# Kernel optimization log

Hardware: AMD Instinct MI355X
Metric: run time of the kernel (lower is better)

The kernel has to match this reference:

```python
import jax, jax.numpy as jnp
import numpy as np

C, H2, E, SQ, SK, HW = 256, 256, 512, 2048, 64, 256

def setup_inputs() -> dict:
    key = jax.random.key(0)
    ks = jax.random.split(key, 12)
    s = 0.05
    return {
        "Z": jax.random.normal(ks[0], (C, HW, HW), jnp.float32),
        "Q": jax.random.normal(ks[1], (SQ, 3), jnp.float32),
        "q_z": jax.random.normal(ks[2], (SQ, C), jnp.float32),
        "r": jax.random.uniform(ks[3], (SQ, SK, 2), jnp.float32) * (HW - 2),
        "w1": jax.random.normal(ks[4], (H2, 2), jnp.float32) * s,
        "b1": jnp.zeros((H2,), jnp.float32),
        "w2": jax.random.normal(ks[5], (H2, 3), jnp.float32) * s,
        "b2": jnp.zeros((H2,), jnp.float32),
        "in_proj_w": jax.random.normal(ks[6], (3 * E, E), jnp.float32) * s,
        "in_proj_b": jnp.zeros((3 * E,), jnp.float32),
        "out_proj_w": jax.random.normal(ks[7], (E, E), jnp.float32) * s,
        "out_proj_b": jnp.zeros((E,), jnp.float32),
        "num_heads": 8,
    }

def bilinear_interpolation_3d(Z, x, y):
    # Z: [c, H, W]; x, y: [N] float coords. Faithful to torch: .int() trunc (coords >= 0)
    c = Z.shape[0]
    x1 = x.astype(jnp.int32)
    y1 = y.astype(jnp.int32)
    x2 = x1 + 1
    y2 = y1 + 1
    Q11 = Z[:, x1, y1]  # [c, N]
    Q12 = Z[:, x1, y2]
    Q21 = Z[:, x2, y1]
    Q22 = Z[:, x2, y2]
    dx = x - x1
    dy = y - y1
    R1 = Q11 * (1 - dx) + Q21 * dx
    R2 = Q12 * (1 - dx) + Q22 * dx
    interp = R1 * (1 - dy) + R2 * dy  # [c, N]
    # faithful to the original: raw row-major reshape (NOT a transpose)
    return jnp.reshape(interp, (-1, c))

def reference(Z, Q, q_z, r, w1, b1, w2, b2, in_proj_w, in_proj_b, out_proj_w, out_proj_b, num_heads):
    size_q, size_k, _ = r.shape
    qr = r.reshape(-1, 2)
    Zr = bilinear_interpolation_3d(Z, qr[:, 0], qr[:, 1])
    Zr = Zr.reshape(size_q, size_k, -1)  # [sq, sk, c]
    r_proj = r @ w1.T + b1               # [sq, sk, h2]
    key = jnp.concatenate([Zr, r_proj], axis=2)  # [sq, sk, E]
    value = key
    q_proj = Q @ w2.T + b2               # [sq, h2]
    query = jnp.concatenate([q_z, q_proj], axis=1)  # [sq, E]
    E_ = query.shape[1]
    hd = E_ // num_heads
    # torch MultiheadAttention in-projection
    ql = query @ in_proj_w[:E_].T + in_proj_b[:E_]              # [sq, E]
    kl = key @ in_proj_w[E_:2 * E_].T + in_proj_b[E_:2 * E_]    # [sq, sk, E]
    vl = value @ in_proj_w[2 * E_:].T + in_proj_b[2 * E_:]
    qh = ql.reshape(size_q, num_heads, hd)
    kh = kl.reshape(size_q, size_k, num_heads, hd)
    vh = vl.reshape(size_q, size_k, num_heads, hd)
    scores = jnp.einsum('bhd,bkhd->bhk', qh, kh) / jnp.sqrt(jnp.asarray(hd, qh.dtype))
    attn = jax.nn.softmax(scores, axis=-1)  # [sq, h, sk]
    out = jnp.einsum('bhk,bkhd->bhd', attn, vh).reshape(size_q, E_)
    out = out @ out_proj_w.T + out_proj_b
    return jnp.concatenate([q_z, out], axis=1)  # [sq, c + E]
```

## Files before the change

### kernel.cpp

```cpp
#include <hip/hip_runtime.h>


typedef _Float16 half8 __attribute__((ext_vector_type(8)));
typedef _Float16 half4v __attribute__((ext_vector_type(4)));
typedef _Float16 half2v __attribute__((ext_vector_type(2)));
typedef float f32x4 __attribute__((ext_vector_type(4)));

#define O_WQT   0u
#define O_WKT   262144u
#define O_WVT   524288u
#define O_WO    786432u
#define O_QRY   1048576u
#define O_WCT   2097152u
#define O_MT    4194304u
#define O_U     6291456u
#define O_G     14680064u
#define O_ZT    23068672u
#define O_ZR    39845888u
#define O_F32   73400320u

__global__ __launch_bounds__(256) void k_pre(
    const float* __restrict__ Z, const float* __restrict__ ipw,
    const float* __restrict__ opw, const float* __restrict__ q_z,
    const float* __restrict__ Qm, const float* __restrict__ w2,
    const float* __restrict__ b2, const float* __restrict__ ipb,
    const float* __restrict__ opb,
    _Float16* __restrict__ wsh, float* __restrict__ bu, float* __restrict__ b_eff)
{
    __shared__ __align__(16) float sbuf[8448];
    int b = blockIdx.x, t = threadIdx.x;

    if (b < 2048) {
        float (*sT)[33] = (float(*)[33])sbuf;
        int x = b >> 3, yt = (b & 7) * 32;
#pragma unroll
        for (int i = 0; i < 8; ++i) {
            int g = i * 256 + t;
            int c = g >> 3, y = (g & 7) * 4;
            float4 v = *(const float4*)(Z + (size_t)c * 65536 + x * 256 + yt + y);
            sT[c][y] = v.x; sT[c][y + 1] = v.y; sT[c][y + 2] = v.z; sT[c][y + 3] = v.w;
        }
        __syncthreads();
        _Float16* Zt = wsh + O_ZT;
        int c4 = (t & 63) * 4;
#pragma unroll
        for (int i = 0; i < 8; ++i) {
            int y = (t >> 6) * 8 + i;
            half4v o;
#pragma unroll
            for (int j = 0; j < 4; ++j) o[j] = (_Float16)sT[c4 + j][y];
            *(half4v*)(Zt + ((size_t)(x * 256 + yt + y)) * 256 + c4) = o;
        }
    } else if (b < 2240) {
        float (*sT)[65] = (float(*)[65])sbuf;
        int bx = b - 2048;
        int sec = bx >> 6, tile = bx & 63;
        int th = tile >> 3, tl = tile & 7;
        int row0, col0;
        if (sec == 0) { row0 = tl * 64;             col0 = th * 64; }
        else          { row0 = 512 * sec + th * 64; col0 = tl * 64; }
        const float* src = ipw + (size_t)row0 * 512 + col0;
#pragma unroll
        for (int i = 0; i < 4; ++i) {
            int rr = i * 16 + (t >> 4), cc = (t & 15) * 4;
            float4 v = *(const float4*)(src + (size_t)rr * 512 + cc);
            sT[rr][cc] = v.x; sT[rr][cc + 1] = v.y; sT[rr][cc + 2] = v.z; sT[rr][cc + 3] = v.w;
        }
        __syncthreads();
        float scale = (sec == 1) ? 0.125f : 1.0f;
#pragma unroll
        for (int it = 0; it < 2; ++it) {
            int g = t + it * 256;
            int a = g >> 3, b8 = (g & 7) * 8;
            half8 o;
#pragma unroll
            for (int j = 0; j < 8; ++j) o[j] = (_Float16)(scale * sT[b8 + j][a]);
            size_t dst;
            if (sec == 0)      dst = O_WQT + (size_t)(th * 64 + a) * 512 + tl * 64 + b8;
            else if (sec == 1) dst = O_WKT + (size_t)th * 32768 + (size_t)(tl * 64 + a) * 64 + b8;
            else               dst = O_WVT + (size_t)th * 32768 + (size_t)(tl * 64 + a) * 64 + b8;
            *(half8*)(wsh + dst) = o;
        }
    } else if (b < 3264) {
        int e4 = ((b - 2240) * 256 + t) * 4;
        int q = e4 >> 9, j = e4 & 511;
        half4v o;
        if (j < 256) {
            float4 v = *(const float4*)(q_z + q * 256 + j);
            o[0] = (_Float16)v.x; o[1] = (_Float16)v.y;
            o[2] = (_Float16)v.z; o[3] = (_Float16)v.w;
        } else {
            float q0 = Qm[q * 3], q1 = Qm[q * 3 + 1], q2 = Qm[q * 3 + 2];
#pragma unroll
            for (int u = 0; u < 4; ++u) {
                int m = j - 256 + u;
                o[u] = (_Float16)(q0 * w2[m * 3] + q1 * w2[m * 3 + 1] + q2 * w2[m * 3 + 2] + b2[m]);
            }
        }
        *(half4v*)(wsh + O_QRY + e4) = o;
    } else if (b < 3520) {
        int e4 = ((b - 3264) * 256 + t) * 4;
        float4 v = *(const float4*)(opw + e4);
        half4v o;
        o[0] = (_Float16)v.x; o[1] = (_Float16)v.y; o[2] = (_Float16)v.z; o[3] = (_Float16)v.w;
        *(half4v*)(wsh + O_WO + e4) = o;
    } else if (b < 3536) {
        int c = (b - 3520) * 256 + t;
        int h = c >> 9, j = c & 511;
        float s = 0.f;
#pragma unroll 4
        for (int d = 0; d < 64; ++d)
            s += ipb[512 + (h << 6) + d] * ipw[(size_t)(512 + (h << 6) + d) * 512 + j];
        bu[c] = 0.125f * s;
    } else {
        int e = (b - 3536) * 4 + (t >> 6), l = t & 63;
        const float* worow = opw + (size_t)e * 512;
        float s = 0.f;
#pragma unroll
        for (int i = 0; i < 8; ++i)
            s += ipb[1024 + l + 64 * i] * worow[l + 64 * i];
#pragma unroll
        for (int mm = 1; mm < 64; mm <<= 1) s += __shfl_xor(s, mm, 64);
        if (l == 0) b_eff[e] = s + opb[e];
    }
}

__global__ __launch_bounds__(256) void k_small2(_Float16* __restrict__ wsh)
{
    __shared__ __align__(16) _Float16 sA[64][72];
    int bx = blockIdx.x;
    int job = bx >> 6, g6 = bx & 63;
    int rb = g6 & 7, h = g6 >> 3;
    int t = threadIdx.x, w = t >> 6, l = t & 63;
    const _Float16* A0 = wsh + (job ? O_WO : O_WQT) + (size_t)rb * 64 * 512 + h * 64;
    const _Float16* B0 = wsh + (job ? O_WVT : O_WKT) + (size_t)h * 512 * 64;
#pragma unroll
    for (int i = 0; i < 2; ++i) {
        int g = t + i * 256;
        int row = g >> 3, colg = (g & 7) * 8;
        *(half8*)&sA[row][colg] = *(const half8*)(A0 + (size_t)row * 512 + colg);
    }
    __syncthreads();
    f32x4 acc[4][8] = {};
    int arow = l & 15, kg = (l >> 4) << 3;
#pragma unroll
    for (int kk = 0; kk < 64; kk += 32) {
        half8 a[4], bb[8];
#pragma unroll
        for (int mt = 0; mt < 4; ++mt) a[mt] = *(const half8*)&sA[mt * 16 + arow][kk + kg];
#pragma unroll
        for (int nt = 0; nt < 8; ++nt) {
            int col = (w << 7) + nt * 16 + arow;
            bb[nt] = *(const half8*)(B0 + (size_t)col * 64 + kk + kg);
        }
#pragma unroll
        for (int mt = 0; mt < 4; ++mt)
#pragma unroll
            for (int nt = 0; nt < 8; ++nt)
                acc[mt][nt] = __builtin_amdgcn_mfma_f32_16x16x32_f16(a[mt], bb[nt], acc[mt][nt], 0, 0, 0);
    }
    if (job == 0) {
        _Float16* C = wsh + O_WCT;
#pragma unroll
        for (int mt = 0; mt < 4; ++mt)
#pragma unroll
            for (int nt = 0; nt < 8; ++nt) {
                int col = (h << 9) + (w << 7) + nt * 16 + arow;
                int row0 = rb * 64 + mt * 16 + ((l >> 4) << 2);
#pragma unroll
                for (int v = 0; v < 4; ++v)
                    C[(size_t)col * 512 + row0 + v] = (_Float16)acc[mt][nt][v];
            }
    } else {
        _Float16* C0 = wsh + O_MT + (size_t)rb * 64 * 4096 + h * 512;
#pragma unroll
        for (int mt = 0; mt < 4; ++mt)
#pragma unroll
            for (int nt = 0; nt < 8; ++nt)
#pragma unroll
                for (int v = 0; v < 4; ++v) {
                    int row = mt * 16 + ((l >> 4) << 2) + v;
                    int col = (w << 7) + nt * 16 + arow;
                    C0[(size_t)row * 4096 + col] = (_Float16)acc[mt][nt][v];
                }
    }
}

__global__ __launch_bounds__(256, 4) void k_mid(
    const float* __restrict__ r, _Float16* __restrict__ wsh,
    const float* __restrict__ bu)
{
    __shared__ __align__(16) unsigned char smem[33792];
    int b = blockIdx.x, t = threadIdx.x, w = t >> 6, l = t & 63;

    if (b < 512) {
        _Float16 (*sA)[264] = (_Float16(*)[264])smem;
        const _Float16* A = wsh + O_QRY;
        const _Float16* B = wsh + O_WCT;
        _Float16* U = wsh + O_U;
        int q0 = (b & 31) * 64;
        int colb = (b >> 5) * 256 + w * 64;
        f32x4 acc[4][4] = {};
        int arow = l & 15, kg = (l >> 4) << 3;
#pragma unroll
        for (int half = 0; half < 2; ++half) {
#pragma unroll
            for (int i = 0; i < 8; ++i) {
                int e = i * 2048 + t * 8;
                *(half8*)&sA[e >> 8][e & 255] =
                    *(const half8*)(A + (size_t)(q0 + (e >> 8)) * 512 + half * 256 + (e & 255));
            }
            __syncthreads();
#pragma unroll 2
            for (int kk = 0; kk < 256; kk += 32) {
                half8 a[4], bb[4];
#pragma unroll
                for (int mt = 0; mt < 4; ++mt) a[mt] = *(const half8*)&sA[mt * 16 + arow][kk + kg];
#pragma unroll
                for (int nt = 0; nt < 4; ++nt)
                    bb[nt] = *(const half8*)(B + (size_t)(colb + nt * 16 + arow) * 512 + half * 256 + kk + kg);
#pragma unroll
                for (int mt = 0; mt < 4; ++mt)
#pragma unroll
                    for (int nt = 0; nt < 4; ++nt)
                        acc[mt][nt] = __builtin_amdgcn_mfma_f32_16x16x32_f16(a[mt], bb[nt], acc[mt][nt], 0, 0, 0);
            }
            __syncthreads();
        }
#pragma unroll
        for (int mt = 0; mt < 4; ++mt)
#pragma unroll
            for (int nt = 0; nt < 4; ++nt)
#pragma unroll
                for (int v = 0; v < 4; ++v) {
                    int row = q0 + mt * 16 + ((l >> 4) << 2) + v;
                    int col = colb + nt * 16 + arow;
                    U[(size_t)row * 4096 + col] = (_Float16)(acc[mt][nt][v] + bu[col]);
                }
    } else {
        float (*sT)[33] = (float(*)[33])smem;
        const _Float16* Zt = wsh + O_ZT;
        _Float16* Zr = wsh + O_ZR;
        int pb = b - 512;
        const float2* r2 = (const float2*)r;
#pragma unroll 2
        for (int i = 0; i < 8; ++i) {
            int ptl = w * 8 + i;
            float2 rv = r2[pb * 32 + ptl];
            int x1 = (int)rv.x, y1 = (int)rv.y;
            float dx = rv.x - (float)x1, dy = rv.y - (float)y1;
            float w11 = (1.f - dx) * (1.f - dy), w21 = dx * (1.f - dy);
            float w12 = (1.f - dx) * dy,         w22 = dx * dy;
            const _Float16* base = Zt + ((size_t)(x1 * 256 + y1)) * 256;
#pragma unroll
            for (int cg = 0; cg < 2; ++cg) {
                int c = cg * 128 + l * 2;
                half2v z11 = *(const half2v*)(base + c);
                half2v z12 = *(const half2v*)(base + 256 + c);
                half2v z21 = *(const half2v*)(base + 65536 + c);
                half2v z22 = *(const half2v*)(base + 65536 + 256 + c);
                sT[c][ptl]     = w11 * (float)z11[0] + w21 * (float)z21[0]
                               + w12 * (float)z12[0] + w22 * (float)z22[0];
                sT[c + 1][ptl] = w11 * (float)z11[1] + w21 * (float)z21[1]
                               + w12 * (float)z12[1] + w22 * (float)z22[1];
            }
        }
        __syncthreads();
        int ch0 = t >> 2, colc = (t & 3) * 8;
#pragma unroll
        for (int g = 0; g < 4; ++g) {
            int ch = g * 64 + ch0;
            half8 o;
#pragma unroll
            for (int j = 0; j < 8; ++j) o[j] = (_Float16)sT[ch][colc + j];
            *(half8*)(Zr + (size_t)ch * 131072 + pb * 32 + colc) = o;
        }
    }
}

__global__ __launch_bounds__(512, 2) void k_main(
    const _Float16* __restrict__ Zr, const float* __restrict__ r,
    const float* __restrict__ w1, const float* __restrict__ b1,
    const _Float16* __restrict__ U, _Float16* __restrict__ G)
{
    __shared__ __align__(16) _Float16 sKey[64][520];
    __shared__ __align__(16) _Float16 sU[8][520];
    __shared__ float sP[512];
    __shared__ float sP2[512];
    __shared__ __align__(16) _Float16 sA16[16][72];

    int q = blockIdx.x;
    int t = threadIdx.x, w = t >> 6, l = t & 63;
    int ch = q >> 3, s8 = q & 7;

    for (int i = t; i < 576; i += 512) ((unsigned*)sA16)[i] = 0u;

    const _Float16* src = Zr + ((size_t)ch * 2048 + s8 * 256) * 64;
#pragma unroll
    for (int i = 0; i < 4; ++i) {
        int e = i * 4096 + t * 8;
        *(half8*)&sKey[e >> 8][e & 255] = *(const half8*)(src + e);
    }
    {
        int e = t * 8;
        *(half8*)&sU[e >> 9][e & 511] = *(const half8*)(U + (size_t)q * 4096 + e);
    }
    {
        int m = t & 255, half = t >> 8;
        float w10 = w1[2 * m], w11 = w1[2 * m + 1], b1m = b1[m];
        const float2* r2q = (const float2*)r + (size_t)q * 64;
#pragma unroll 8
        for (int i = 0; i < 32; ++i) {
            int k = half * 32 + i;
            float2 rv = r2q[k];
            sKey[k][256 + m] = (_Float16)(rv.x * w10 + rv.y * w11 + b1m);
        }
    }
    __syncthreads();

    {
        f32x4 acc = {};
        int arow = l & 15, kg = (l >> 4) << 3;
        int wm = w & 3, khalf = (w >> 2) << 8;
        const _Float16* ar = &sKey[wm * 16 + arow][khalf + kg];
        const _Float16* br = &sU[l & 7][khalf + kg];
#pragma unroll
        for (int kk = 0; kk < 256; kk += 32)
            acc = __builtin_amdgcn_mfma_f32_16x16x32_f16(
                *(const half8*)(ar + kk), *(const half8*)(br + kk), acc, 0, 0, 0);
        if ((l & 15) < 8) {
            int h = l & 15, krow0 = wm * 16 + ((l >> 4) << 2);
            float* dst = (w < 4) ? sP : sP2;
#pragma unroll
            for (int v = 0; v < 4; ++v) dst[(h << 6) + krow0 + v] = acc[v];
        }
    }
    __syncthreads();

    {
        float v = sP[t] + sP2[t];
        float mx = v;
#pragma unroll
        for (int mm = 1; mm < 64; mm <<= 1) mx = fmaxf(mx, __shfl_xor(mx, mm, 64));
        float e = __expf(v - mx);
        float sm = e;
#pragma unroll
        for (int mm = 1; mm < 64; mm <<= 1) sm += __shfl_xor(sm, mm, 64);
        sA16[w][l] = (_Float16)(e / sm);
    }
    __syncthreads();

    {
        f32x4 acc[4] = {};
        int arow = l & 15, kq = (l >> 4) << 3;
        half8 a0 = *(const half8*)&sA16[arow][kq];
        half8 a1 = *(const half8*)&sA16[arow][32 + kq];
#pragma unroll
        for (int nt = 0; nt < 4; ++nt) {
            int n0 = (w << 6) + (nt << 4);
            half8 b0, b1f;
#pragma unroll
            for (int jj = 0; jj < 8; ++jj) b0[jj] = sKey[kq + jj][n0 + arow];
            acc[nt] = __builtin_amdgcn_mfma_f32_16x16x32_f16(a0, b0, acc[nt], 0, 0, 0);
#pragma unroll
            for (int jj = 0; jj < 8; ++jj) b1f[jj] = sKey[32 + kq + jj][n0 + arow];
            acc[nt] = __builtin_amdgcn_mfma_f32_16x16x32_f16(a1, b1f, acc[nt], 0, 0, 0);
        }
        if (l < 32) {
            int rgrp = (l >> 4) << 2;
#pragma unroll
            for (int nt = 0; nt < 4; ++nt) {
                int n0 = (w << 6) + (nt << 4);
#pragma unroll
                for (int v = 0; v < 4; ++v)
                    sU[rgrp + v][n0 + arow] = (_Float16)acc[nt][v];
            }
        }
    }
    __syncthreads();

    {
        int c = t * 8;
        *(half8*)(G + (size_t)q * 4096 + c) = *(const half8*)&sU[c >> 9][c & 511];
    }
}

__global__ __launch_bounds__(256) void k_final(
    const _Float16* __restrict__ G, const _Float16* __restrict__ Mt,
    const float* __restrict__ b_eff, const float* __restrict__ qz,
    float* __restrict__ out)
{
    __shared__ __align__(16) _Float16 sA[64][520];
    int rb = blockIdx.x, cb = blockIdx.y;
    int q0 = rb * 64;
    int t = threadIdx.x, w = t >> 6, l = t & 63;

    if (cb == 0) {
#pragma unroll
        for (int i = 0; i < 16; ++i) {
            int idx4 = i * 256 + t;
            int row = idx4 >> 6, c = (idx4 & 63) << 2;
            *(float4*)&out[(size_t)(q0 + row) * 768 + c] =
                *(const float4*)&qz[(size_t)(q0 + row) * 256 + c];
        }
    }

    f32x4 acc[4][2] = {};
    int arow = l & 15, kg = (l >> 4) << 3;
    int e0 = cb * 128 + (w << 5);
    for (int c = 0; c < 8; ++c) {
#pragma unroll
        for (int i = 0; i < 16; ++i) {
            int e = i * 2048 + t * 8;
            *(half8*)&sA[e >> 9][e & 511] =
                *(const half8*)(G + (size_t)(q0 + (e >> 9)) * 4096 + c * 512 + (e & 511));
        }
        __syncthreads();
#pragma unroll 4
        for (int kk = 0; kk < 512; kk += 32) {
            half8 a[4], bb[2];
#pragma unroll
            for (int nt = 0; nt < 2; ++nt)
                bb[nt] = *(const half8*)(Mt + (size_t)(e0 + nt * 16 + arow) * 4096 + c * 512 + kk + kg);
#pragma unroll
            for (int mt = 0; mt < 4; ++mt) {
                a[mt] = *(const half8*)&sA[mt * 16 + arow][kk + kg];
#pragma unroll
                for (int nt = 0; nt < 2; ++nt)
                    acc[mt][nt] = __builtin_amdgcn_mfma_f32_16x16x32_f16(a[mt], bb[nt], acc[mt][nt], 0, 0, 0);
            }
        }
        __syncthreads();
    }
#pragma unroll
    for (int mt = 0; mt < 4; ++mt)
#pragma unroll
        for (int nt = 0; nt < 2; ++nt)
#pragma unroll
            for (int v = 0; v < 4; ++v) {
                int row = q0 + mt * 16 + ((l >> 4) << 2) + v;
                int ecol = e0 + nt * 16 + arow;
                out[(size_t)row * 768 + 256 + ecol] = acc[mt][nt][v] + b_eff[ecol];
            }
}

extern "C" void kernel_launch(void* const* d_in, const int* in_sizes, int n_in,
                              void* d_out, int out_size, void* d_ws, size_t ws_size,
                              hipStream_t stream) {
    const float* Z          = (const float*)d_in[0];
    const float* Qm         = (const float*)d_in[1];
    const float* q_z        = (const float*)d_in[2];
    const float* r          = (const float*)d_in[3];
    const float* w1         = (const float*)d_in[4];
    const float* b1         = (const float*)d_in[5];
    const float* w2         = (const float*)d_in[6];
    const float* b2         = (const float*)d_in[7];
    const float* in_proj_w  = (const float*)d_in[8];
    const float* in_proj_b  = (const float*)d_in[9];
    const float* out_proj_w = (const float*)d_in[10];
    const float* out_proj_b = (const float*)d_in[11];
    float* out = (float*)d_out;

    _Float16* wsh = (_Float16*)d_ws;
    _Float16* Mt    = wsh + O_MT;
    _Float16* U     = wsh + O_U;
    _Float16* G     = wsh + O_G;
    _Float16* Zr    = wsh + O_ZR;
    float*    bu    = (float*)(wsh + O_F32);
    float*    b_eff = bu + 4096;

    k_pre<<<3664, 256, 0, stream>>>(Z, in_proj_w, out_proj_w, q_z, Qm, w2, b2,
                                    in_proj_b, out_proj_b, wsh, bu, b_eff);
    k_small2<<<128, 256, 0, stream>>>(wsh);
    k_mid<<<4608, 256, 0, stream>>>(r, wsh, bu);
    k_main<<<2048, 512, 0, stream>>>(Zr, r, w1, b1, U, G);
    k_final<<<dim3(32, 4), 256, 0, stream>>>(G, Mt, b_eff, q_z, out);
}
```

Measured before the change: 281.4 us.

## Fuse weight-product GEMMs into preprocessing, retile mid/final kernels for occupancy

Drops the separate weight transpose/convert stage and the k_small2 kernel. k_pre now computes the combined Wq·Wk and Wo·Wv products directly from the fp32 weights in shared-memory tiles, which removes one launch and its intermediate buffers. k_mid's GEMM tiles shrink from 64 to 32 rows, launch bounds rise to 6 blocks, and the bilinear gather now does 8-channel vector loads and stages the result in fp16 in LDS. k_final uses 32-row tiles so twice as many blocks run. The smaller tiles reread more weight data in exchange for more parallelism, and fusing the weight GEMM into k_pre may make those blocks heavier.

```diff
diff --git a/kernel.cpp b/kernel.cpp
--- a/kernel.cpp
+++ b/kernel.cpp
@@ -3,13 +3,8 @@
 
 typedef _Float16 half8 __attribute__((ext_vector_type(8)));
 typedef _Float16 half4v __attribute__((ext_vector_type(4)));
-typedef _Float16 half2v __attribute__((ext_vector_type(2)));
 typedef float f32x4 __attribute__((ext_vector_type(4)));
 
-#define O_WQT   0u
-#define O_WKT   262144u
-#define O_WVT   524288u
-#define O_WO    786432u
 #define O_QRY   1048576u
 #define O_WCT   2097152u
 #define O_MT    4194304u
@@ -27,7 +22,7 @@
     const float* __restrict__ opb,
     _Float16* __restrict__ wsh, float* __restrict__ bu, float* __restrict__ b_eff)
 {
-    __shared__ __align__(16) float sbuf[8448];
+    __shared__ __align__(16) unsigned char sbuf[33792];
     int b = blockIdx.x, t = threadIdx.x;
 
     if (b < 2048) {
@@ -51,38 +46,8 @@
             for (int j = 0; j < 4; ++j) o[j] = (_Float16)sT[c4 + j][y];
             *(half4v*)(Zt + ((size_t)(x * 256 + yt + y)) * 256 + c4) = o;
         }
-    } else if (b < 2240) {
-        float (*sT)[65] = (float(*)[65])sbuf;
-        int bx = b - 2048;
-        int sec = bx >> 6, tile = bx & 63;
-        int th = tile >> 3, tl = tile & 7;
-        int row0, col0;
-        if (sec == 0) { row0 = tl * 64;             col0 = th * 64; }
-        else          { row0 = 512 * sec + th * 64; col0 = tl * 64; }
-        const float* src = ipw + (size_t)row0 * 512 + col0;
-#pragma unroll
-        for (int i = 0; i < 4; ++i) {
-            int rr = i * 16 + (t >> 4), cc = (t & 15) * 4;
-            float4 v = *(const float4*)(src + (size_t)rr * 512 + cc);
-            sT[rr][cc] = v.x; sT[rr][cc + 1] = v.y; sT[rr][cc + 2] = v.z; sT[rr][cc + 3] = v.w;
-        }
-        __syncthreads();
-        float scale = (sec == 1) ? 0.125f : 1.0f;
-#pragma unroll
-        for (int it = 0; it < 2; ++it) {
-            int g = t + it * 256;
-            int a = g >> 3, b8 = (g & 7) * 8;
-            half8 o;
-#pragma unroll
-            for (int j = 0; j < 8; ++j) o[j] = (_Float16)(scale * sT[b8 + j][a]);
-            size_t dst;
-            if (sec == 0)      dst = O_WQT + (size_t)(th * 64 + a) * 512 + tl * 64 + b8;
-            else if (sec == 1) dst = O_WKT + (size_t)th * 32768 + (size_t)(tl * 64 + a) * 64 + b8;
-            else               dst = O_WVT + (size_t)th * 32768 + (size_t)(tl * 64 + a) * 64 + b8;
-            *(half8*)(wsh + dst) = o;
-        }
-    } else if (b < 3264) {
-        int e4 = ((b - 2240) * 256 + t) * 4;
+    } else if (b < 3072) {
+        int e4 = ((b - 2048) * 256 + t) * 4;
         int q = e4 >> 9, j = e4 & 511;
         half4v o;
         if (j < 256) {
@@ -98,14 +63,75 @@
             }
         }
         *(half4v*)(wsh + O_QRY + e4) = o;
-    } else if (b < 3520) {
-        int e4 = ((b - 3264) * 256 + t) * 4;
-        float4 v = *(const float4*)(opw + e4);
-        half4v o;
-        o[0] = (_Float16)v.x; o[1] = (_Float16)v.y; o[2] = (_Float16)v.z; o[3] = (_Float16)v.w;
-        *(half4v*)(wsh + O_WO + e4) = o;
-    } else if (b < 3536) {
-        int c = (b - 3520) * 256 + t;
+    } else if (b < 4096) {
+        int isMt = (b >= 3584);
+        int b2 = b - (isMt ? 3584 : 3072);
+        int h = b2 >> 6, jt = (b2 >> 3) & 7, lt = b2 & 7;
+        _Float16 (*sAm)[72] = (_Float16(*)[72])sbuf;
+        _Float16 (*sBn)[72] = (_Float16(*)[72])(sbuf + 9216);
+        int j0 = jt * 64, l0 = lt * 64;
+        int dd = t >> 4, c4 = (t & 15) * 4;
+#pragma unroll
+        for (int ii = 0; ii < 4; ++ii) {
+            int d = ii * 16 + dd;
+            if (!isMt) {
+                float4 k4 = *(const float4*)(ipw + (size_t)(512 + h * 64 + d) * 512 + j0 + c4);
+                float4 q4 = *(const float4*)(ipw + (size_t)(h * 64 + d) * 512 + l0 + c4);
+                sAm[c4 + 0][d] = (_Float16)(0.125f * k4.x);
+                sAm[c4 + 1][d] = (_Float16)(0.125f * k4.y);
+                sAm[c4 + 2][d] = (_Float16)(0.125f * k4.z);
+                sAm[c4 + 3][d] = (_Float16)(0.125f * k4.w);
+                sBn[c4 + 0][d] = (_Float16)q4.x;
+                sBn[c4 + 1][d] = (_Float16)q4.y;
+                sBn[c4 + 2][d] = (_Float16)q4.z;
+                sBn[c4 + 3][d] = (_Float16)q4.w;
+            } else {
+                int e = ii * 16 + dd;
+                float4 o4 = *(const float4*)(opw + (size_t)(l0 + e) * 512 + h * 64 + c4);
+                half4v ov;
+                ov[0] = (_Float16)o4.x; ov[1] = (_Float16)o4.y;
+                ov[2] = (_Float16)o4.z; ov[3] = (_Float16)o4.w;
+                *(half4v*)&sAm[e][c4] = ov;
+                float4 v4 = *(const float4*)(ipw + (size_t)(1024 + h * 64 + d) * 512 + j0 + c4);
+                sBn[c4 + 0][d] = (_Float16)v4.x;
+                sBn[c4 + 1][d] = (_Float16)v4.y;
+                sBn[c4 + 2][d] = (_Float16)v4.z;
+                sBn[c4 + 3][d] = (_Float16)v4.w;
+            }
+        }
+        __syncthreads();
+        int w = t >> 6, l = t & 63;
+        int arow = l & 15, kg = (l >> 4) << 3;
+        f32x4 acc[4] = {};
+#pragma unroll
+        for (int kk = 0; kk < 64; kk += 32) {
+            half8 a = *(const half8*)&sAm[w * 16 + arow][kk + kg];
+#pragma unroll
+            for (int nt = 0; nt < 4; ++nt) {
+                half8 bb = *(const half8*)&sBn[nt * 16 + arow][kk + kg];
+                acc[nt] = __builtin_amdgcn_mfma_f32_16x16x32_f16(a, bb, acc[nt], 0, 0, 0);
+            }
+        }
+        int rg = (l >> 4) << 2;
+        if (!isMt) {
+            _Float16* Wc = wsh + O_WCT;
+#pragma unroll
+            for (int nt = 0; nt < 4; ++nt)
+#pragma unroll
+                for (int v = 0; v < 4; ++v)
+                    Wc[(size_t)(h * 512 + j0 + w * 16 + rg + v) * 512 + l0 + nt * 16 + arow] =
+                        (_Float16)acc[nt][v];
+        } else {
+            _Float16* Mt = wsh + O_MT;
+#pragma unroll
+            for (int nt = 0; nt < 4; ++nt)
+#pragma unroll
+                for (int v = 0; v < 4; ++v)
+                    Mt[(size_t)(l0 + w * 16 + rg + v) * 4096 + h * 512 + j0 + nt * 16 + arow] =
+                        (_Float16)acc[nt][v];
+        }
+    } else if (b < 4112) {
+        int c = (b - 4096) * 256 + t;
         int h = c >> 9, j = c & 511;
         float s = 0.f;
 #pragma unroll 4
@@ -113,7 +139,7 @@
             s += ipb[512 + (h << 6) + d] * ipw[(size_t)(512 + (h << 6) + d) * 512 + j];
         bu[c] = 0.125f * s;
     } else {
-        int e = (b - 3536) * 4 + (t >> 6), l = t & 63;
+        int e = (b - 4112) * 4 + (t >> 6), l = t & 63;
         const float* worow = opw + (size_t)e * 512;
         float s = 0.f;
 #pragma unroll
@@ -125,102 +151,41 @@
     }
 }
 
-__global__ __launch_bounds__(256) void k_small2(_Float16* __restrict__ wsh)
-{
-    __shared__ __align__(16) _Float16 sA[64][72];
-    int bx = blockIdx.x;
-    int job = bx >> 6, g6 = bx & 63;
-    int rb = g6 & 7, h = g6 >> 3;
-    int t = threadIdx.x, w = t >> 6, l = t & 63;
-    const _Float16* A0 = wsh + (job ? O_WO : O_WQT) + (size_t)rb * 64 * 512 + h * 64;
-    const _Float16* B0 = wsh + (job ? O_WVT : O_WKT) + (size_t)h * 512 * 64;
-#pragma unroll
-    for (int i = 0; i < 2; ++i) {
-        int g = t + i * 256;
-        int row = g >> 3, colg = (g & 7) * 8;
-        *(half8*)&sA[row][colg] = *(const half8*)(A0 + (size_t)row * 512 + colg);
-    }
-    __syncthreads();
-    f32x4 acc[4][8] = {};
-    int arow = l & 15, kg = (l >> 4) << 3;
-#pragma unroll
-    for (int kk = 0; kk < 64; kk += 32) {
-        half8 a[4], bb[8];
-#pragma unroll
-        for (int mt = 0; mt < 4; ++mt) a[mt] = *(const half8*)&sA[mt * 16 + arow][kk + kg];
-#pragma unroll
-        for (int nt = 0; nt < 8; ++nt) {
-            int col = (w << 7) + nt * 16 + arow;
-            bb[nt] = *(const half8*)(B0 + (size_t)col * 64 + kk + kg);
-        }
-#pragma unroll
-        for (int mt = 0; mt < 4; ++mt)
-#pragma unroll
-            for (int nt = 0; nt < 8; ++nt)
-                acc[mt][nt] = __builtin_amdgcn_mfma_f32_16x16x32_f16(a[mt], bb[nt], acc[mt][nt], 0, 0, 0);
-    }
-    if (job == 0) {
-        _Float16* C = wsh + O_WCT;
-#pragma unroll
-        for (int mt = 0; mt < 4; ++mt)
-#pragma unroll
-            for (int nt = 0; nt < 8; ++nt) {
-                int col = (h << 9) + (w << 7) + nt * 16 + arow;
-                int row0 = rb * 64 + mt * 16 + ((l >> 4) << 2);
-#pragma unroll
-                for (int v = 0; v < 4; ++v)
-                    C[(size_t)col * 512 + row0 + v] = (_Float16)acc[mt][nt][v];
-            }
-    } else {
-        _Float16* C0 = wsh + O_MT + (size_t)rb * 64 * 4096 + h * 512;
-#pragma unroll
-        for (int mt = 0; mt < 4; ++mt)
-#pragma unroll
-            for (int nt = 0; nt < 8; ++nt)
-#pragma unroll
-                for (int v = 0; v < 4; ++v) {
-                    int row = mt * 16 + ((l >> 4) << 2) + v;
-                    int col = (w << 7) + nt * 16 + arow;
-                    C0[(size_t)row * 4096 + col] = (_Float16)acc[mt][nt][v];
-                }
-    }
-}
-
-__global__ __launch_bounds__(256, 4) void k_mid(
+__global__ __launch_bounds__(256, 6) void k_mid(
     const float* __restrict__ r, _Float16* __restrict__ wsh,
     const float* __restrict__ bu)
 {
-    __shared__ __align__(16) unsigned char smem[33792];
+    __shared__ __align__(16) unsigned char smem[16896];
     int b = blockIdx.x, t = threadIdx.x, w = t >> 6, l = t & 63;
 
-    if (b < 512) {
-        _Float16 (*sA)[264] = (_Float16(*)[264])smem;
+    if (b < 1024) {
+        _Float16 (*sA)[136] = (_Float16(*)[136])smem;
         const _Float16* A = wsh + O_QRY;
         const _Float16* B = wsh + O_WCT;
         _Float16* U = wsh + O_U;
-        int q0 = (b & 31) * 64;
-        int colb = (b >> 5) * 256 + w * 64;
-        f32x4 acc[4][4] = {};
+        int q0 = (b & 63) * 32;
+        int colb = (b >> 6) * 256 + w * 64;
+        f32x4 acc[2][4] = {};
         int arow = l & 15, kg = (l >> 4) << 3;
 #pragma unroll
-        for (int half = 0; half < 2; ++half) {
-#pragma unroll
-            for (int i = 0; i < 8; ++i) {
+        for (int s = 0; s < 4; ++s) {
+#pragma unroll
+            for (int i = 0; i < 2; ++i) {
                 int e = i * 2048 + t * 8;
-                *(half8*)&sA[e >> 8][e & 255] =
-                    *(const half8*)(A + (size_t)(q0 + (e >> 8)) * 512 + half * 256 + (e & 255));
+                *(half8*)&sA[e >> 7][e & 127] =
+                    *(const half8*)(A + (size_t)(q0 + (e >> 7)) * 512 + s * 128 + (e & 127));
             }
             __syncthreads();
-#pragma unroll 2
-            for (int kk = 0; kk < 256; kk += 32) {
-                half8 a[4], bb[4];
-#pragma unroll
-                for (int mt = 0; mt < 4; ++mt) a[mt] = *(const half8*)&sA[mt * 16 + arow][kk + kg];
+#pragma unroll
+            for (int kk = 0; kk < 128; kk += 32) {
+                half8 a[2], bb[4];
+#pragma unroll
+                for (int mt = 0; mt < 2; ++mt) a[mt] = *(const half8*)&sA[mt * 16 + arow][kk + kg];
 #pragma unroll
                 for (int nt = 0; nt < 4; ++nt)
-                    bb[nt] = *(const half8*)(B + (size_t)(colb + nt * 16 + arow) * 512 + half * 256 + kk + kg);
-#pragma unroll
-                for (int mt = 0; mt < 4; ++mt)
+                    bb[nt] = *(const half8*)(B + (size_t)(colb + nt * 16 + arow) * 512 + s * 128 + kk + kg);
+#pragma unroll
+                for (int mt = 0; mt < 2; ++mt)
 #pragma unroll
                     for (int nt = 0; nt < 4; ++nt)
                         acc[mt][nt] = __builtin_amdgcn_mfma_f32_16x16x32_f16(a[mt], bb[nt], acc[mt][nt], 0, 0, 0);
@@ -228,7 +193,7 @@
             __syncthreads();
         }
 #pragma unroll
-        for (int mt = 0; mt < 4; ++mt)
+        for (int mt = 0; mt < 2; ++mt)
 #pragma unroll
             for (int nt = 0; nt < 4; ++nt)
 #pragma unroll
@@ -238,42 +203,41 @@
                     U[(size_t)row * 4096 + col] = (_Float16)(acc[mt][nt][v] + bu[col]);
                 }
     } else {
-        float (*sT)[33] = (float(*)[33])smem;
+        _Float16 (*sT)[264] = (_Float16(*)[264])smem;
         const _Float16* Zt = wsh + O_ZT;
         _Float16* Zr = wsh + O_ZR;
-        int pb = b - 512;
+        int pb = b - 1024;
         const float2* r2 = (const float2*)r;
-#pragma unroll 2
-        for (int i = 0; i < 8; ++i) {
-            int ptl = w * 8 + i;
+        int hb = l >> 5, ch0 = (l & 31) * 8;
+#pragma unroll
+        for (int i = 0; i < 4; ++i) {
+            int ptl = i * 8 + w * 2 + hb;
             float2 rv = r2[pb * 32 + ptl];
             int x1 = (int)rv.x, y1 = (int)rv.y;
             float dx = rv.x - (float)x1, dy = rv.y - (float)y1;
             float w11 = (1.f - dx) * (1.f - dy), w21 = dx * (1.f - dy);
             float w12 = (1.f - dx) * dy,         w22 = dx * dy;
-            const _Float16* base = Zt + ((size_t)(x1 * 256 + y1)) * 256;
-#pragma unroll
-            for (int cg = 0; cg < 2; ++cg) {
-                int c = cg * 128 + l * 2;
-                half2v z11 = *(const half2v*)(base + c);
-                half2v z12 = *(const half2v*)(base + 256 + c);
-                half2v z21 = *(const half2v*)(base + 65536 + c);
-                half2v z22 = *(const half2v*)(base + 65536 + 256 + c);
-                sT[c][ptl]     = w11 * (float)z11[0] + w21 * (float)z21[0]
-                               + w12 * (float)z12[0] + w22 * (float)z22[0];
-                sT[c + 1][ptl] = w11 * (float)z11[1] + w21 * (float)z21[1]
-                               + w12 * (float)z12[1] + w22 * (float)z22[1];
-            }
+            const _Float16* base = Zt + ((size_t)(x1 * 256 + y1)) * 256 + ch0;
+            half8 z11 = *(const half8*)(base);
+            half8 z12 = *(const half8*)(base + 256);
+            half8 z21 = *(const half8*)(base + 65536);
+            half8 z22 = *(const half8*)(base + 65536 + 256);
+            half8 o;
+#pragma unroll
+            for (int c = 0; c < 8; ++c)
+                o[c] = (_Float16)(w11 * (float)z11[c] + w21 * (float)z21[c]
+                                + w12 * (float)z12[c] + w22 * (float)z22[c]);
+            *(half8*)&sT[ptl][ch0] = o;
         }
         __syncthreads();
-        int ch0 = t >> 2, colc = (t & 3) * 8;
+        int ch_ = t >> 2, pt8 = (t & 3) * 8;
 #pragma unroll
         for (int g = 0; g < 4; ++g) {
-            int ch = g * 64 + ch0;
+            int ch = g * 64 + ch_;
             half8 o;
 #pragma unroll
-            for (int j = 0; j < 8; ++j) o[j] = (_Float16)sT[ch][colc + j];
-            *(half8*)(Zr + (size_t)ch * 131072 + pb * 32 + colc) = o;
+            for (int j = 0; j < 8; ++j) o[j] = sT[pt8 + j][ch];
+            *(half8*)(Zr + (size_t)ch * 131072 + pb * 32 + pt8) = o;
         }
     }
 }
@@ -390,14 +354,14 @@
     const float* __restrict__ b_eff, const float* __restrict__ qz,
     float* __restrict__ out)
 {
-    __shared__ __align__(16) _Float16 sA[64][520];
+    __shared__ __align__(16) _Float16 sA[32][520];
     int rb = blockIdx.x, cb = blockIdx.y;
-    int q0 = rb * 64;
+    int q0 = rb * 32;
     int t = threadIdx.x, w = t >> 6, l = t & 63;
 
     if (cb == 0) {
 #pragma unroll
-        for (int i = 0; i < 16; ++i) {
+        for (int i = 0; i < 8; ++i) {
             int idx4 = i * 256 + t;
             int row = idx4 >> 6, c = (idx4 & 63) << 2;
             *(float4*)&out[(size_t)(q0 + row) * 768 + c] =
@@ -405,12 +369,12 @@
         }
     }
 
-    f32x4 acc[4][2] = {};
+    f32x4 acc[2][2] = {};
     int arow = l & 15, kg = (l >> 4) << 3;
     int e0 = cb * 128 + (w << 5);
     for (int c = 0; c < 8; ++c) {
 #pragma unroll
-        for (int i = 0; i < 16; ++i) {
+        for (int i = 0; i < 8; ++i) {
             int e = i * 2048 + t * 8;
             *(half8*)&sA[e >> 9][e & 511] =
                 *(const half8*)(G + (size_t)(q0 + (e >> 9)) * 4096 + c * 512 + (e & 511));
@@ -418,12 +382,12 @@
         __syncthreads();
 #pragma unroll 4
         for (int kk = 0; kk < 512; kk += 32) {
-            half8 a[4], bb[2];
+            half8 a[2], bb[2];
 #pragma unroll
             for (int nt = 0; nt < 2; ++nt)
                 bb[nt] = *(const half8*)(Mt + (size_t)(e0 + nt * 16 + arow) * 4096 + c * 512 + kk + kg);
 #pragma unroll
-            for (int mt = 0; mt < 4; ++mt) {
+            for (int mt = 0; mt < 2; ++mt) {
                 a[mt] = *(const half8*)&sA[mt * 16 + arow][kk + kg];
 #pragma unroll
                 for (int nt = 0; nt < 2; ++nt)
@@ -433,7 +397,7 @@
         __syncthreads();
     }
 #pragma unroll
-    for (int mt = 0; mt < 4; ++mt)
+    for (int mt = 0; mt < 2; ++mt)
 #pragma unroll
         for (int nt = 0; nt < 2; ++nt)
 #pragma unroll
@@ -469,10 +433,9 @@
     float*    bu    = (float*)(wsh + O_F32);
     float*    b_eff = bu + 4096;
 
-    k_pre<<<3664, 256, 0, stream>>>(Z, in_proj_w, out_proj_w, q_z, Qm, w2, b2,
+    k_pre<<<4240, 256, 0, stream>>>(Z, in_proj_w, out_proj_w, q_z, Qm, w2, b2,
                                     in_proj_b, out_proj_b, wsh, bu, b_eff);
-    k_small2<<<128, 256, 0, stream>>>(wsh);
-    k_mid<<<4608, 256, 0, stream>>>(r, wsh, bu);
+    k_mid<<<5120, 256, 0, stream>>>(r, wsh, bu);
     k_main<<<2048, 512, 0, stream>>>(Zr, r, w1, b1, U, G);
-    k_final<<<dim3(32, 4), 256, 0, stream>>>(G, Mt, b_eff, q_z, out);
+    k_final<<<dim3(64, 4), 256, 0, stream>>>(G, Mt, b_eff, q_z, out);
 }
```

After: 288.6 us. +2.6%, slower.
